# Performance work log

Measured on AMD Instinct MI355X. Metric: run time of the kernel, lower is better.

The kernel has to match this reference:

```python
import jax, jax.numpy as jnp
import numpy as np

B, L, E, H = 4, 2048, 512, 8
D = E // H
FACTOR = 5
U = min(FACTOR * int(np.ceil(np.log(L))), L)  # sample_k == n_top == 40


def setup_inputs() -> dict:
    key0 = jax.random.key(0)
    ks = jax.random.split(key0, 12)
    s = 0.02
    inp = {
        "query": jax.random.normal(ks[0], (B, L, E), jnp.float32),
        "key": jax.random.normal(ks[1], (B, L, E), jnp.float32),
        "value": jax.random.normal(ks[2], (B, L, E), jnp.float32),
        "index_sample": jax.random.randint(ks[3], (L, U), 0, L, jnp.int32),
    }
    for i, nm in enumerate(["q", "k", "v", "o"]):
        inp[f"W{nm}"] = jax.random.normal(ks[4 + i], (E, E), jnp.float32) * s
        inp[f"b{nm}"] = jnp.zeros((E,), jnp.float32)
    return inp


def reference(query, key, value, index_sample, Wq, bq, Wk, bk, Wv, bv, Wo, bo):
    # projections (nn.Linear: x @ W.T + b)
    q = (query @ Wq.T + bq).reshape(B, L, H, D).transpose(0, 2, 1, 3)  # [B,H,L,D]
    k = (key @ Wk.T + bk).reshape(B, L, H, D).transpose(0, 2, 1, 3)
    v = (value @ Wv.T + bv).reshape(B, L, H, D).transpose(0, 2, 1, 3)

    L_Q = L_K = L
    sample_k = index_sample.shape[1]
    n_top = min(sample_k, L_Q)

    # --- _prob_QK: sampled QK scores, note: NO 1/sqrt(D) scaling in source ---
    K_sample = k[:, :, index_sample, :]                      # [B,H,L_Q,sample_k,D]
    QK_sample = jnp.einsum('bhld,bhlsd->bhls', q, K_sample)  # [B,H,L_Q,sample_k]
    M = QK_sample.max(axis=-1) - QK_sample.sum(axis=-1) / L_K
    _, M_top = jax.lax.top_k(M, n_top)                       # [B,H,n_top]
    Q_reduce = jnp.take_along_axis(q, M_top[..., None], axis=2)  # [B,H,n_top,D]
    scores = jnp.einsum('bhud,bhkd->bhuk', Q_reduce, k)      # [B,H,n_top,L_K]

    # --- initial context (eval mode: mean of V) ---
    context = jnp.broadcast_to(v.mean(axis=2, keepdims=True), (B, H, L_Q, D))

    # --- update context at selected queries ---
    attn = jax.nn.softmax(scores, axis=-1)
    upd = jnp.einsum('bhuk,bhkd->bhud', attn, v)             # [B,H,n_top,D]
    bi = jnp.arange(B)[:, None, None]
    hi = jnp.arange(H)[None, :, None]
    context = context.at[bi, hi, M_top].set(upd)

    out = context.transpose(0, 2, 1, 3).reshape(B, L, E) @ Wo.T + bo
    return out
```

## Files before the change

kernel.cpp:

```cpp
#include <hip/hip_runtime.h>
#include <hip/hip_bf16.h>
#include <math.h>

constexpr int BB = 4;
constexpr int LL = 2048;
constexpr int EE = 512;
constexpr int HH = 8;
constexpr int DD = 64;
constexpr int UU = 40;
constexpr int NT = 40;
constexpr int NCH = 32;
constexpr int CK = 64;
constexpr int MVC = 16;
constexpr float NEG_INF = -3.0e38f;

typedef __attribute__((ext_vector_type(8))) short bf8_t;
typedef __attribute__((ext_vector_type(4))) float f4_t;

__device__ __forceinline__ void split2(float x, uint& h, uint& m)
{
    uint  xb = __float_as_uint(x);
    uint  hb = (xb + 0x7fffu + ((xb >> 16) & 1u)) & 0xffff0000u;
    float r  = x - __uint_as_float(hb);
    h = hb >> 16;
    m = (__float_as_uint(r) & 0xffff0000u) >> 16;
}

__device__ __forceinline__ void split2pair(float x0, float x1, uint& hp, uint& mp)
{
    uint xb0 = __float_as_uint(x0), xb1 = __float_as_uint(x1);
    uint hb0 = xb0 + 0x7fffu + ((xb0 >> 16) & 1u);
    uint hb1 = xb1 + 0x7fffu + ((xb1 >> 16) & 1u);
    hp = __builtin_amdgcn_perm(hb1, hb0, 0x07060302u);
    float r0 = x0 - __uint_as_float(hb0 & 0xffff0000u);
    float r1 = x1 - __uint_as_float(hb1 & 0xffff0000u);
    mp = __builtin_amdgcn_perm(__float_as_uint(r1), __float_as_uint(r0), 0x07060302u);
}

__device__ __forceinline__ void gload16(const void* g, void* l)
{
    __builtin_amdgcn_global_load_lds(
        (const __attribute__((address_space(1))) unsigned int*)g,
        (__attribute__((address_space(3))) unsigned int*)l, 16, 0, 0);
}

__device__ __forceinline__ int swz(int row, int c)
{
    return row * 64 + (((c ^ row ^ (row >> 2)) & 3) << 4);
}

__global__ __launch_bounds__(256) void wconv_kernel(
    const float* __restrict__ Wq, const float* __restrict__ Wk,
    const float* __restrict__ Wv, unsigned short* __restrict__ wcv)
{
    const int gi  = blockIdx.x * 256 + threadIdx.x;
    const int z   = gi >> 15;
    const int off = (gi & 32767) * 8;
    const float* W = (z == 0) ? Wq : (z == 1 ? Wk : Wv);
    float x[8];
    *(float4*)(x)     = *(const float4*)(W + off);
    *(float4*)(x + 4) = *(const float4*)(W + off + 4);
    uint hp[4], mp[4];
#pragma unroll
    for (int p = 0; p < 4; p++) split2pair(x[2 * p], x[2 * p + 1], hp[p], mp[p]);
    unsigned short* Wh = wcv + (size_t)z * 524288;
    *(uint4*)(Wh + off)          = make_uint4(hp[0], hp[1], hp[2], hp[3]);
    *(uint4*)(Wh + 262144 + off) = make_uint4(mp[0], mp[1], mp[2], mp[3]);
}

__global__ __launch_bounds__(256, 3) void proj_kernel(
    const float* __restrict__ Xq, const float* __restrict__ Xk, const float* __restrict__ Xv,
    const unsigned short* __restrict__ Wcv,
    const float* __restrict__ bq, const float* __restrict__ bk, const float* __restrict__ bv,
    float* __restrict__ Oq, float* __restrict__ Ok, float* __restrict__ Ov)
{
    const int bid = blockIdx.x;
    const int xg  = bid & 7;
    const int s   = bid >> 3;
    const int yz  = xg * 24 + (s >> 2);
    const int zi  = yz >> 6;
    const int yi  = yz & 63;
    const int m0  = yi * 128;
    const int n0  = (s & 3) * 128;

    const float* X; const float* bias; float* O;
    if (zi == 0)      { X = Xq; bias = bq; O = Oq; }
    else if (zi == 1) { X = Xk; bias = bk; O = Ok; }
    else              { X = Xv; bias = bv; O = Ov; }
    const unsigned short* Wh = Wcv + (size_t)zi * 524288;
    const unsigned short* Wm = Wh + 262144;

    __shared__ char ldsmem[49152];
    char* const LA = ldsmem;
    char* const LB = ldsmem + 16384;

    const int tid  = threadIdx.x;
    const int lane = tid & 63;
    const int wave = tid >> 6;

    const int srow  = tid >> 1;
    const int shalf = tid & 1;
    const int w0 = swz(srow, shalf * 2);
    const int w1 = swz(srow, shalf * 2 + 1);
    const float* Aptr = X + (size_t)(m0 + srow) * EE + shalf * 16;

    const int r0 = tid >> 2;
    const int r1 = 64 + r0;
    const int c0 = (tid & 3) ^ ((r0 ^ (r0 >> 2)) & 3);
    const int c1 = (tid & 3) ^ ((r1 ^ (r1 >> 2)) & 3);
    const unsigned short* bh0 = Wh + (size_t)(n0 + r0) * EE + c0 * 8;
    const unsigned short* bh1 = Wh + (size_t)(n0 + r1) * EE + c1 * 8;
    const unsigned short* bm0 = Wm + (size_t)(n0 + r0) * EE + c0 * 8;
    const unsigned short* bm1 = Wm + (size_t)(n0 + r1) * EE + c1 * 8;
    const int ldst = tid * 16;

    const int rxor = ((((lane >> 4) ^ lane ^ (lane >> 2)) & 3) << 4);
    const int arow = (wave >> 1) * 64 + (lane & 15);
    const int brow = (wave & 1) * 64 + (lane & 15);

    f4_t acc[4][4];
#pragma unroll
    for (int i = 0; i < 4; i++)
#pragma unroll
        for (int j = 0; j < 4; j++) acc[i][j] = (f4_t)0.0f;

    float fa[16];
#pragma unroll
    for (int q = 0; q < 4; q++)
        *(float4*)(fa + q * 4) = *(const float4*)(Aptr + q * 4);
    gload16(bh0, LB + ldst);
    gload16(bh1, LB + 4096 + ldst);
    gload16(bm0, LB + 8192 + ldst);
    gload16(bm1, LB + 12288 + ldst);

    int parity = 0;
#pragma unroll 2
    for (int kt = 0; kt < EE; kt += 32) {
        uint ahu[8], amu[8];
#pragma unroll
        for (int p = 0; p < 8; p++)
            split2pair(fa[2 * p], fa[2 * p + 1], ahu[p], amu[p]);

        __syncthreads();
        *(uint4*)(LA +    0 + w0) = make_uint4(ahu[0], ahu[1], ahu[2], ahu[3]);
        *(uint4*)(LA +    0 + w1) = make_uint4(ahu[4], ahu[5], ahu[6], ahu[7]);
        *(uint4*)(LA + 8192 + w0) = make_uint4(amu[0], amu[1], amu[2], amu[3]);
        *(uint4*)(LA + 8192 + w1) = make_uint4(amu[4], amu[5], amu[6], amu[7]);
        __syncthreads();

        if (kt + 32 < EE) {
            const int kn = kt + 32;
#pragma unroll
            for (int q = 0; q < 4; q++)
                *(float4*)(fa + q * 4) = *(const float4*)(Aptr + kn + q * 4);
            char* Bn = LB + (parity ^ 1) * 16384;
            gload16(bh0 + kn, Bn + ldst);
            gload16(bh1 + kn, Bn + 4096 + ldst);
            gload16(bm0 + kn, Bn + 8192 + ldst);
            gload16(bm1 + kn, Bn + 12288 + ldst);
        }

        char* const Bb = LB + parity * 16384;
        bf8_t af[4][2];
#pragma unroll
        for (int i = 0; i < 4; i++) {
            const int ro = (arow + i * 16) * 64 + rxor;
            af[i][0] = *(const bf8_t*)(LA +    0 + ro);
            af[i][1] = *(const bf8_t*)(LA + 8192 + ro);
        }
#pragma unroll
        for (int j = 0; j < 4; j++) {
            const int ro = (brow + j * 16) * 64 + rxor;
            bf8_t bh_ = *(const bf8_t*)(Bb +    0 + ro);
            bf8_t bm_ = *(const bf8_t*)(Bb + 8192 + ro);
#pragma unroll
            for (int i = 0; i < 4; i++) {
                f4_t c = acc[i][j];
                c = __builtin_amdgcn_mfma_f32_16x16x32_bf16(af[i][0], bh_, c, 0, 0, 0);
                c = __builtin_amdgcn_mfma_f32_16x16x32_bf16(af[i][0], bm_, c, 0, 0, 0);
                c = __builtin_amdgcn_mfma_f32_16x16x32_bf16(af[i][1], bh_, c, 0, 0, 0);
                acc[i][j] = c;
            }
        }
        parity ^= 1;
    }

#pragma unroll
    for (int j = 0; j < 4; j++) {
        const int n  = n0 + (wave & 1) * 64 + j * 16 + (lane & 15);
        const float bn = bias[n];
        const int h_ = n >> 6, d_ = n & 63;
#pragma unroll
        for (int i = 0; i < 4; i++) {
            const int mb = m0 + (wave >> 1) * 64 + i * 16 + ((lane >> 4) << 2);
#pragma unroll
            for (int r = 0; r < 4; r++) {
                const int m  = mb + r;
                const int b_ = m >> 11;
                const int l_ = m & (LL - 1);
                O[(((size_t)(b_ * HH + h_) * LL + l_) << 6) + d_] = acc[i][j][r] + bn;
            }
        }
    }
}

__global__ __launch_bounds__(256) void meanv_part_kernel(const float* __restrict__ v,
                                                         float* __restrict__ vpart)
{
    const int bh    = blockIdx.x & 31;
    const int chunk = blockIdx.x >> 5;
    const int d  = threadIdx.x & 63;
    const int wv = threadIdx.x >> 6;
    const float* base = v + ((size_t)bh * LL + chunk * 128 + wv * 32) * DD + d;
    float acc = 0.0f;
#pragma unroll
    for (int i = 0; i < 32; i++) acc += base[i * DD];
    __shared__ float red[4][DD];
    red[wv][d] = acc;
    __syncthreads();
    if (wv == 0)
        vpart[(size_t)(chunk * 32 + bh) * DD + d]
            = red[0][d] + red[1][d] + red[2][d] + red[3][d];
}

__global__ __launch_bounds__(64) void meanv_comb_kernel(const float* __restrict__ vpart,
                                                        float* __restrict__ mean_v)
{
    const int bh = blockIdx.x;
    const int d  = threadIdx.x;
    float s = 0.0f;
#pragma unroll
    for (int c = 0; c < MVC; c++) s += vpart[(size_t)(c * 32 + bh) * DD + d];
    mean_v[bh * DD + d] = s * (1.0f / (float)LL);
}

__global__ __launch_bounds__(256) void measure_kernel(const float* __restrict__ q,
                                                      const float* __restrict__ k,
                                                      const int* __restrict__ idx_sample,
                                                      float* __restrict__ M)
{
    int bh   = blockIdx.x & 31;
    int lc   = blockIdx.x >> 5;
    int lane = threadIdx.x & 63;
    int wv   = threadIdx.x >> 6;
    int l    = lc * 4 + wv;
    int s8   = lane >> 3;
    int c    = lane & 7;

    const float* qrow = q + ((size_t)bh * LL + l) * DD + c * 8;
    float4 q0 = *(const float4*)(qrow);
    float4 q1 = *(const float4*)(qrow + 4);

    const float* kbase = k + (size_t)bh * LL * DD;
    const int*   irow  = idx_sample + l * UU;

    float mx = NEG_INF, sum = 0.0f;
#pragma unroll
    for (int it = 0; it < UU; it += 8) {
        int ki = irow[it + s8];
        const float* krow = kbase + (size_t)ki * DD + c * 8;
        float4 k0 = *(const float4*)(krow);
        float4 k1 = *(const float4*)(krow + 4);
        float p = q0.x*k0.x + q0.y*k0.y + q0.z*k0.z + q0.w*k0.w
                + q1.x*k1.x + q1.y*k1.y + q1.z*k1.z + q1.w*k1.w;
        p += __shfl_xor(p, 1, 64);
        p += __shfl_xor(p, 2, 64);
        p += __shfl_xor(p, 4, 64);
        mx = fmaxf(mx, p);
        sum += p;
    }
    mx  = fmaxf(mx, __shfl_xor(mx, 8, 64));
    sum += __shfl_xor(sum, 8, 64);
    mx  = fmaxf(mx, __shfl_xor(mx, 16, 64));
    sum += __shfl_xor(sum, 16, 64);
    mx  = fmaxf(mx, __shfl_xor(mx, 32, 64));
    sum += __shfl_xor(sum, 32, 64);

    if (lane == 0) M[bh * LL + l] = mx - sum * (1.0f / (float)LL);
}

__global__ __launch_bounds__(64) void topk_kernel(const float* __restrict__ M,
                                                  int* __restrict__ top)
{
    const int bh   = blockIdx.x;
    const int lane = threadIdx.x;

    unsigned long long keys[32];
#pragma unroll
    for (int i = 0; i < 32; i++) {
        int idx = i * 64 + lane;
        uint u  = __float_as_uint(M[bh * LL + idx]);
        uint sv = (u & 0x80000000u) ? ~u : (u | 0x80000000u);
        keys[i] = ((unsigned long long)sv << 32) | (uint)(LL - 1 - idx);
    }
    unsigned long long lmax = 0ull;
#pragma unroll
    for (int i = 0; i < 32; i++) lmax = (keys[i] > lmax) ? keys[i] : lmax;

    for (int it = 0; it < NT; it++) {
        unsigned long long g = lmax;
#pragma unroll
        for (int off = 1; off < 64; off <<= 1) {
            unsigned long long o = __shfl_xor(g, off, 64);
            g = (o > g) ? o : g;
        }
        if (lane == 0) top[bh * NT + it] = LL - 1 - (int)(g & 0xffffffffu);
#pragma unroll
        for (int i = 0; i < 32; i++) if (keys[i] == g) keys[i] = 0ull;
        lmax = 0ull;
#pragma unroll
        for (int i = 0; i < 32; i++) lmax = (keys[i] > lmax) ? keys[i] : lmax;
    }
}

__global__ __launch_bounds__(256) void pv_kernel(const float* __restrict__ q,
                                                 const float* __restrict__ k,
                                                 const float* __restrict__ v,
                                                 const int* __restrict__ top,
                                                 float* __restrict__ mpart,
                                                 float* __restrict__ lpart,
                                                 float* __restrict__ accpart)
{
    const int bh    = blockIdx.x & 31;
    const int chunk = blockIdx.x >> 5;
    const int tid   = threadIdx.x;
    const int lane  = tid & 63, wv = tid >> 6;

    __shared__ alignas(16) float qs[NT][DD];
    __shared__ alignas(16) float sc[NT][CK + 4];

    for (int i = tid; i < NT * DD / 4; i += 256) {
        int u  = i >> 4;
        int d4 = (i & 15) * 4;
        int l  = top[bh * NT + u];
        *(float4*)&qs[u][d4] = *(const float4*)(q + ((size_t)bh * LL + l) * DD + d4);
    }
    __syncthreads();

    {
        const int key  = tid >> 2;
        const int dseg = tid & 3;
        const float* krow = k + ((size_t)bh * LL + chunk * CK + key) * DD + dseg * 16;
        float4 k0 = *(const float4*)(krow);
        float4 k1 = *(const float4*)(krow + 4);
        float4 k2 = *(const float4*)(krow + 8);
        float4 k3 = *(const float4*)(krow + 12);
#pragma unroll 8
        for (int u = 0; u < NT; u++) {
            const float* qrow = &qs[u][dseg * 16];
            float4 q0 = *(const float4*)(qrow);
            float4 q1 = *(const float4*)(qrow + 4);
            float4 q2 = *(const float4*)(qrow + 8);
            float4 q3 = *(const float4*)(qrow + 12);
            float p = k0.x*q0.x + k0.y*q0.y + k0.z*q0.z + k0.w*q0.w
                    + k1.x*q1.x + k1.y*q1.y + k1.z*q1.z + k1.w*q1.w
                    + k2.x*q2.x + k2.y*q2.y + k2.z*q2.z + k2.w*q2.w
                    + k3.x*q3.x + k3.y*q3.y + k3.z*q3.z + k3.w*q3.w;
            p += __shfl_xor(p, 1, 64);
            p += __shfl_xor(p, 2, 64);
            if (dseg == 0) sc[u][key] = p;
        }
    }
    __syncthreads();

#pragma unroll
    for (int i = 0; i < 10; i++) {
        const int u = wv * 10 + i;
        float val = sc[u][lane];
        float mx = val;
        mx = fmaxf(mx, __shfl_xor(mx, 1, 64));
        mx = fmaxf(mx, __shfl_xor(mx, 2, 64));
        mx = fmaxf(mx, __shfl_xor(mx, 4, 64));
        mx = fmaxf(mx, __shfl_xor(mx, 8, 64));
        mx = fmaxf(mx, __shfl_xor(mx, 16, 64));
        mx = fmaxf(mx, __shfl_xor(mx, 32, 64));
        float e = __expf(val - mx);
        sc[u][lane] = e;
        float s = e;
        s += __shfl_xor(s, 1, 64);
        s += __shfl_xor(s, 2, 64);
        s += __shfl_xor(s, 4, 64);
        s += __shfl_xor(s, 8, 64);
        s += __shfl_xor(s, 16, 64);
        s += __shfl_xor(s, 32, 64);
        if (lane == 0) {
            mpart[(bh * NCH + chunk) * NT + u] = mx;
            lpart[(bh * NCH + chunk) * NT + u] = s;
        }
    }
    __syncthreads();

    {
        float pacc[10];
#pragma unroll
        for (int i = 0; i < 10; i++) pacc[i] = 0.0f;
        const float* vbase = v + ((size_t)bh * LL + chunk * CK) * DD + lane;
#pragma unroll 4
        for (int t = 0; t < CK; t += 4) {
            float v0 = vbase[(size_t)(t + 0) * DD];
            float v1 = vbase[(size_t)(t + 1) * DD];
            float v2 = vbase[(size_t)(t + 2) * DD];
            float v3 = vbase[(size_t)(t + 3) * DD];
#pragma unroll
            for (int i = 0; i < 10; i++) {
                float4 s = *(const float4*)&sc[wv * 10 + i][t];
                pacc[i] += s.x * v0 + s.y * v1 + s.z * v2 + s.w * v3;
            }
        }
#pragma unroll
        for (int i = 0; i < 10; i++) {
            const int u = wv * 10 + i;
            accpart[(((size_t)(bh * NCH + chunk)) * NT + u) * 64 + lane] = pacc[i];
        }
    }
}

__global__ __launch_bounds__(256) void base_kernel(const float* __restrict__ mean_v,
                                                   const float* __restrict__ Wo,
                                                   const float* __restrict__ bo,
                                                   float* __restrict__ base)
{
    int lane = threadIdx.x & 63, wv = threadIdx.x >> 6;
    int be = blockIdx.x * 4 + wv;
    int b  = be >> 9;
    int e  = be & (EE - 1);
    const float* mrow = mean_v + b * EE;
    const float* wrow = Wo + (size_t)e * EE;
    float acc = 0.0f;
#pragma unroll
    for (int j = 0; j < 8; j++) acc += mrow[lane + j * 64] * wrow[lane + j * 64];
#pragma unroll
    for (int off = 32; off > 0; off >>= 1) acc += __shfl_down(acc, off, 64);
    if (lane == 0) base[be] = acc + bo[e];
}

__global__ __launch_bounds__(256) void bcast_kernel(const float* __restrict__ base,
                                                    float* __restrict__ out)
{
    size_t fi = ((size_t)blockIdx.x * 256 + threadIdx.x) * 4;
    int b  = (int)(fi >> 20);
    int e4 = (int)(fi & (EE - 1));
    float4 val = *(const float4*)(base + b * EE + e4);
    *(float4*)(out + fi) = val;
}

__global__ __launch_bounds__(256) void corr_kernel(const float* __restrict__ accpart,
                                                   const float* __restrict__ lpart,
                                                   const float* __restrict__ mpart,
                                                   const float* __restrict__ mean_v,
                                                   const int* __restrict__ top,
                                                   const float* __restrict__ Wo,
                                                   float* __restrict__ out)
{
    int bhu = blockIdx.x;
    int bh  = bhu / NT;
    int u   = bhu % NT;
    int h   = bh & (HH - 1);
    int b   = bh >> 3;
    int tid = threadIdx.x;
    int l   = top[bhu];

    __shared__ float delta[DD];
    if (tid < DD) {
        float m = NEG_INF;
#pragma unroll 8
        for (int c = 0; c < NCH; c++) m = fmaxf(m, mpart[(bh * NCH + c) * NT + u]);
        float den = 0.0f, num = 0.0f;
#pragma unroll 8
        for (int c = 0; c < NCH; c++) {
            float f = __expf(mpart[(bh * NCH + c) * NT + u] - m);
            den += lpart[(bh * NCH + c) * NT + u] * f;
            num += accpart[(((size_t)(bh * NCH + c)) * NT + u) * 64 + tid] * f;
        }
        delta[tid] = num / den - mean_v[bh * DD + tid];
    }
    __syncthreads();

    float* orow = out + ((size_t)(b * LL + l)) * EE;
#pragma unroll
    for (int rep = 0; rep < 2; rep++) {
        int e = tid + rep * 256;
        const float* wrow = Wo + (size_t)e * EE + h * DD;
        float acc = 0.0f;
#pragma unroll
        for (int d = 0; d < DD; d++) acc += delta[d] * wrow[d];
        atomicAdd(orow + e, acc);
    }
}

extern "C" void kernel_launch(void* const* d_in, const int* in_sizes, int n_in,
                              void* d_out, int out_size, void* d_ws, size_t ws_size,
                              hipStream_t stream)
{
    const float* query = (const float*)d_in[0];
    const float* key   = (const float*)d_in[1];
    const float* value = (const float*)d_in[2];
    const int*   idxs  = (const int*)d_in[3];
    const float* Wq = (const float*)d_in[4];
    const float* bq = (const float*)d_in[5];
    const float* Wk = (const float*)d_in[6];
    const float* bk = (const float*)d_in[7];
    const float* Wv = (const float*)d_in[8];
    const float* bv = (const float*)d_in[9];
    const float* Wo = (const float*)d_in[10];
    const float* bo = (const float*)d_in[11];
    float* out = (float*)d_out;

    char* ws = (char*)d_ws;
    size_t off = 0;
    const size_t qkv_bytes = (size_t)BB * HH * LL * DD * sizeof(float);
    float* q_ws = (float*)(ws + off); off += qkv_bytes;
    float* k_ws = (float*)(ws + off); off += qkv_bytes;
    float* v_ws = (float*)(ws + off); off += qkv_bytes;
    float* M_ws    = (float*)(ws + off); off += (size_t)BB * HH * LL * sizeof(float);
    int*   top_ws  = (int*)(ws + off);   off += (size_t)BB * HH * NT * sizeof(int);
    float* mean_ws = (float*)(ws + off); off += (size_t)BB * HH * DD * sizeof(float);
    float* vpart_ws = (float*)(ws + off); off += (size_t)BB * HH * MVC * DD * sizeof(float);
    float* mpart_ws = (float*)(ws + off); off += (size_t)BB * HH * NCH * NT * sizeof(float);
    float* lpart_ws = (float*)(ws + off); off += (size_t)BB * HH * NCH * NT * sizeof(float);
    float* accpart_ws = (float*)(ws + off); off += (size_t)BB * HH * NCH * NT * DD * sizeof(float);
    float* base_ws = (float*)(ws + off); off += (size_t)BB * EE * sizeof(float);

    unsigned short* wcv_ws = (unsigned short*)accpart_ws;

    wconv_kernel<<<384, 256, 0, stream>>>(Wq, Wk, Wv, wcv_ws);
    proj_kernel<<<768, 256, 0, stream>>>(query, key, value, wcv_ws, bq, bk, bv,
                                         q_ws, k_ws, v_ws);
    meanv_part_kernel<<<BB * HH * MVC, 256, 0, stream>>>(v_ws, vpart_ws);
    meanv_comb_kernel<<<BB * HH, 64, 0, stream>>>(vpart_ws, mean_ws);
    measure_kernel<<<(LL / 4) * 32, 256, 0, stream>>>(q_ws, k_ws, idxs, M_ws);
    topk_kernel<<<BB * HH, 64, 0, stream>>>(M_ws, top_ws);
    pv_kernel<<<BB * HH * NCH, 256, 0, stream>>>(q_ws, k_ws, v_ws, top_ws,
                                                 mpart_ws, lpart_ws, accpart_ws);
    base_kernel<<<(BB * EE) / 4, 256, 0, stream>>>(mean_ws, Wo, bo, base_ws);
    bcast_kernel<<<(BB * LL * EE) / (256 * 4), 256, 0, stream>>>(base_ws, out);
    corr_kernel<<<BB * HH * NT, 256, 0, stream>>>(accpart_ws, lpart_ws, mpart_ws,
                                                  mean_ws, top_ws, Wo, out);
}
```

Baseline: 316.3 us.

## Double-buffer A tile in LDS and cut to one barrier per K-step

The projection GEMM now double-buffers the converted A tile (bf16 hi/lo split) in LDS alongside B, and prefetches raw A two steps ahead in registers. The A conversion and LDS write for the next step overlap with the MFMAs of the current one. This replaces two __syncthreads per iteration with a single manual waitcnt plus s_barrier. LDS grows to 64KB and launch bounds drop to 2 blocks per CU, which lowers occupancy in exchange for less synchronization stall.

```diff
diff --git a/kernel.cpp b/kernel.cpp
--- a/kernel.cpp
+++ b/kernel.cpp
@@ -17,15 +17,6 @@
 typedef __attribute__((ext_vector_type(8))) short bf8_t;
 typedef __attribute__((ext_vector_type(4))) float f4_t;
 
-__device__ __forceinline__ void split2(float x, uint& h, uint& m)
-{
-    uint  xb = __float_as_uint(x);
-    uint  hb = (xb + 0x7fffu + ((xb >> 16) & 1u)) & 0xffff0000u;
-    float r  = x - __uint_as_float(hb);
-    h = hb >> 16;
-    m = (__float_as_uint(r) & 0xffff0000u) >> 16;
-}
-
 __device__ __forceinline__ void split2pair(float x0, float x1, uint& hp, uint& mp)
 {
     uint xb0 = __float_as_uint(x0), xb1 = __float_as_uint(x1);
@@ -68,7 +59,7 @@
     *(uint4*)(Wh + 262144 + off) = make_uint4(mp[0], mp[1], mp[2], mp[3]);
 }
 
-__global__ __launch_bounds__(256, 3) void proj_kernel(
+__global__ __launch_bounds__(256, 2) void proj_kernel(
     const float* __restrict__ Xq, const float* __restrict__ Xk, const float* __restrict__ Xv,
     const unsigned short* __restrict__ Wcv,
     const float* __restrict__ bq, const float* __restrict__ bk, const float* __restrict__ bv,
@@ -90,9 +81,9 @@
     const unsigned short* Wh = Wcv + (size_t)zi * 524288;
     const unsigned short* Wm = Wh + 262144;
 
-    __shared__ char ldsmem[49152];
-    char* const LA = ldsmem;
-    char* const LB = ldsmem + 16384;
+    __shared__ char ldsmem[65536];
+    char* const LA  = ldsmem;
+    char* const LBt = ldsmem + 32768;
 
     const int tid  = threadIdx.x;
     const int lane = tid & 63;
@@ -124,65 +115,97 @@
 #pragma unroll
         for (int j = 0; j < 4; j++) acc[i][j] = (f4_t)0.0f;
 
-    float fa[16];
-#pragma unroll
-    for (int q = 0; q < 4; q++)
-        *(float4*)(fa + q * 4) = *(const float4*)(Aptr + q * 4);
-    gload16(bh0, LB + ldst);
-    gload16(bh1, LB + 4096 + ldst);
-    gload16(bm0, LB + 8192 + ldst);
-    gload16(bm1, LB + 12288 + ldst);
-
-    int parity = 0;
-#pragma unroll 2
-    for (int kt = 0; kt < EE; kt += 32) {
+    float faA[16], faB[16];
+
+    {
+        float f0[16];
+#pragma unroll
+        for (int q = 0; q < 4; q++)
+            *(float4*)(f0 + q * 4) = *(const float4*)(Aptr + q * 4);
         uint ahu[8], amu[8];
 #pragma unroll
         for (int p = 0; p < 8; p++)
-            split2pair(fa[2 * p], fa[2 * p + 1], ahu[p], amu[p]);
-
-        __syncthreads();
+            split2pair(f0[2 * p], f0[2 * p + 1], ahu[p], amu[p]);
         *(uint4*)(LA +    0 + w0) = make_uint4(ahu[0], ahu[1], ahu[2], ahu[3]);
         *(uint4*)(LA +    0 + w1) = make_uint4(ahu[4], ahu[5], ahu[6], ahu[7]);
         *(uint4*)(LA + 8192 + w0) = make_uint4(amu[0], amu[1], amu[2], amu[3]);
         *(uint4*)(LA + 8192 + w1) = make_uint4(amu[4], amu[5], amu[6], amu[7]);
-        __syncthreads();
-
-        if (kt + 32 < EE) {
-            const int kn = kt + 32;
+        gload16(bh0, LBt + ldst);
+        gload16(bh1, LBt + 4096 + ldst);
+        gload16(bm0, LBt + 8192 + ldst);
+        gload16(bm1, LBt + 12288 + ldst);
+        asm volatile("" ::: "memory");
+#pragma unroll
+        for (int q = 0; q < 4; q++)
+            *(float4*)(faB + q * 4) = *(const float4*)(Aptr + 32 + q * 4);
+        asm volatile("s_waitcnt vmcnt(4) lgkmcnt(0)" ::: "memory");
+        __builtin_amdgcn_s_barrier();
+    }
+
+    auto body = [&](int i, float* fconv, float* fload) {
+        char* const Ab = LA  + ((i & 1) << 14);
+        char* const Bb = LBt + ((i & 1) << 14);
+
+        bf8_t af[4][2];
+#pragma unroll
+        for (int i4 = 0; i4 < 4; i4++) {
+            const int ro = (arow + i4 * 16) * 64 + rxor;
+            af[i4][0] = *(const bf8_t*)(Ab +    0 + ro);
+            af[i4][1] = *(const bf8_t*)(Ab + 8192 + ro);
+        }
+
+        if (i < 15) {
+            uint ahu[8], amu[8];
+#pragma unroll
+            for (int p = 0; p < 8; p++)
+                split2pair(fconv[2 * p], fconv[2 * p + 1], ahu[p], amu[p]);
+            char* const Aw = LA + (((i + 1) & 1) << 14);
+            *(uint4*)(Aw +    0 + w0) = make_uint4(ahu[0], ahu[1], ahu[2], ahu[3]);
+            *(uint4*)(Aw +    0 + w1) = make_uint4(ahu[4], ahu[5], ahu[6], ahu[7]);
+            *(uint4*)(Aw + 8192 + w0) = make_uint4(amu[0], amu[1], amu[2], amu[3]);
+            *(uint4*)(Aw + 8192 + w1) = make_uint4(amu[4], amu[5], amu[6], amu[7]);
+            const int kn = (i + 1) * 32;
+            char* const Bw = LBt + (((i + 1) & 1) << 14);
+            gload16(bh0 + kn, Bw + ldst);
+            gload16(bh1 + kn, Bw + 4096 + ldst);
+            gload16(bm0 + kn, Bw + 8192 + ldst);
+            gload16(bm1 + kn, Bw + 12288 + ldst);
+        }
+        asm volatile("" ::: "memory");
+        if (i < 14) {
+            const int kf = (i + 2) * 32;
 #pragma unroll
             for (int q = 0; q < 4; q++)
-                *(float4*)(fa + q * 4) = *(const float4*)(Aptr + kn + q * 4);
-            char* Bn = LB + (parity ^ 1) * 16384;
-            gload16(bh0 + kn, Bn + ldst);
-            gload16(bh1 + kn, Bn + 4096 + ldst);
-            gload16(bm0 + kn, Bn + 8192 + ldst);
-            gload16(bm1 + kn, Bn + 12288 + ldst);
-        }
-
-        char* const Bb = LB + parity * 16384;
-        bf8_t af[4][2];
-#pragma unroll
-        for (int i = 0; i < 4; i++) {
-            const int ro = (arow + i * 16) * 64 + rxor;
-            af[i][0] = *(const bf8_t*)(LA +    0 + ro);
-            af[i][1] = *(const bf8_t*)(LA + 8192 + ro);
-        }
+                *(float4*)(fload + q * 4) = *(const float4*)(Aptr + kf + q * 4);
+        }
+
 #pragma unroll
         for (int j = 0; j < 4; j++) {
             const int ro = (brow + j * 16) * 64 + rxor;
             bf8_t bh_ = *(const bf8_t*)(Bb +    0 + ro);
             bf8_t bm_ = *(const bf8_t*)(Bb + 8192 + ro);
 #pragma unroll
-            for (int i = 0; i < 4; i++) {
-                f4_t c = acc[i][j];
-                c = __builtin_amdgcn_mfma_f32_16x16x32_bf16(af[i][0], bh_, c, 0, 0, 0);
-                c = __builtin_amdgcn_mfma_f32_16x16x32_bf16(af[i][0], bm_, c, 0, 0, 0);
-                c = __builtin_amdgcn_mfma_f32_16x16x32_bf16(af[i][1], bh_, c, 0, 0, 0);
-                acc[i][j] = c;
+            for (int i4 = 0; i4 < 4; i4++) {
+                f4_t c = acc[i4][j];
+                c = __builtin_amdgcn_mfma_f32_16x16x32_bf16(af[i4][0], bh_, c, 0, 0, 0);
+                c = __builtin_amdgcn_mfma_f32_16x16x32_bf16(af[i4][0], bm_, c, 0, 0, 0);
+                c = __builtin_amdgcn_mfma_f32_16x16x32_bf16(af[i4][1], bh_, c, 0, 0, 0);
+                acc[i4][j] = c;
             }
         }
-        parity ^= 1;
+
+        if (i < 15) {
+            if (i < 14)
+                asm volatile("s_waitcnt vmcnt(4) lgkmcnt(0)" ::: "memory");
+            else
+                asm volatile("s_waitcnt vmcnt(0) lgkmcnt(0)" ::: "memory");
+            __builtin_amdgcn_s_barrier();
+        }
+    };
+
+    for (int it = 0; it < 16; it += 2) {
+        body(it,     faB, faA);
+        body(it + 1, faA, faB);
     }
 
 #pragma unroll
```

Result: no change. 321.6 us (+1.7%).

## Restructure correction kernel to reuse Wo tile across all selected queries per head

Applied to the files above, without the earlier changes.

The correction kernel now runs one block per (batch-head, 128-column slice of output) instead of one block per selected query. Each block combines the partial softmax results for all 40 selected queries into shared memory and stages a 128x64 slice of Wo in LDS, so each Wo element is read once per head rather than once per query. The grid shrinks from 1280 to 128 blocks, which lowers parallelism and adds redundant recombination of partials across the four column slices. The PV inner loop is also changed from a float4 step over four keys to scalar per-key loads with unroll 8.

```diff
diff --git a/kernel.cpp b/kernel.cpp
--- a/kernel.cpp
+++ b/kernel.cpp
@@ -16,15 +16,6 @@
 
 typedef __attribute__((ext_vector_type(8))) short bf8_t;
 typedef __attribute__((ext_vector_type(4))) float f4_t;
-
-__device__ __forceinline__ void split2(float x, uint& h, uint& m)
-{
-    uint  xb = __float_as_uint(x);
-    uint  hb = (xb + 0x7fffu + ((xb >> 16) & 1u)) & 0xffff0000u;
-    float r  = x - __uint_as_float(hb);
-    h = hb >> 16;
-    m = (__float_as_uint(r) & 0xffff0000u) >> 16;
-}
 
 __device__ __forceinline__ void split2pair(float x0, float x1, uint& hp, uint& mp)
 {
@@ -326,8 +317,8 @@
     const int tid   = threadIdx.x;
     const int lane  = tid & 63, wv = tid >> 6;
 
-    __shared__ alignas(16) float qs[NT][DD];
-    __shared__ alignas(16) float sc[NT][CK + 4];
+    __shared__ float qs[NT][DD];
+    __shared__ float sc[NT][CK + 4];
 
     for (int i = tid; i < NT * DD / 4; i += 256) {
         int u  = i >> 4;
@@ -394,18 +385,12 @@
         float pacc[10];
 #pragma unroll
         for (int i = 0; i < 10; i++) pacc[i] = 0.0f;
-        const float* vbase = v + ((size_t)bh * LL + chunk * CK) * DD + lane;
-#pragma unroll 4
-        for (int t = 0; t < CK; t += 4) {
-            float v0 = vbase[(size_t)(t + 0) * DD];
-            float v1 = vbase[(size_t)(t + 1) * DD];
-            float v2 = vbase[(size_t)(t + 2) * DD];
-            float v3 = vbase[(size_t)(t + 3) * DD];
-#pragma unroll
-            for (int i = 0; i < 10; i++) {
-                float4 s = *(const float4*)&sc[wv * 10 + i][t];
-                pacc[i] += s.x * v0 + s.y * v1 + s.z * v2 + s.w * v3;
-            }
+        const float* vbase = v + ((size_t)bh * LL + chunk * CK) * DD;
+#pragma unroll 8
+        for (int t = 0; t < CK; t++) {
+            float vval = vbase[(size_t)t * DD + lane];
+#pragma unroll
+            for (int i = 0; i < 10; i++) pacc[i] += sc[wv * 10 + i][t] * vval;
         }
 #pragma unroll
         for (int i = 0; i < 10; i++) {
@@ -452,39 +437,56 @@
                                                    const float* __restrict__ Wo,
                                                    float* __restrict__ out)
 {
-    int bhu = blockIdx.x;
-    int bh  = bhu / NT;
-    int u   = bhu % NT;
-    int h   = bh & (HH - 1);
-    int b   = bh >> 3;
-    int tid = threadIdx.x;
-    int l   = top[bhu];
-
-    __shared__ float delta[DD];
-    if (tid < DD) {
-        float m = NEG_INF;
+    const int bh  = blockIdx.x & 31;
+    const int ec  = blockIdx.x >> 5;
+    const int h   = bh & (HH - 1);
+    const int b   = bh >> 3;
+    const int tid = threadIdx.x;
+
+    __shared__ float delta[NT][DD + 1];
+    __shared__ float wot[128][DD + 1];
+    __shared__ int   ltab[NT];
+
+    {
+        const int ug = tid >> 6;
+        const int d  = tid & 63;
+        for (int u = ug; u < NT; u += 4) {
+            const float* mp = mpart + (size_t)bh * NCH * NT + u;
+            const float* lp = lpart + (size_t)bh * NCH * NT + u;
+            float m = NEG_INF;
 #pragma unroll 8
-        for (int c = 0; c < NCH; c++) m = fmaxf(m, mpart[(bh * NCH + c) * NT + u]);
-        float den = 0.0f, num = 0.0f;
+            for (int c = 0; c < NCH; c++) m = fmaxf(m, mp[c * NT]);
+            float den = 0.0f, num = 0.0f;
 #pragma unroll 8
-        for (int c = 0; c < NCH; c++) {
-            float f = __expf(mpart[(bh * NCH + c) * NT + u] - m);
-            den += lpart[(bh * NCH + c) * NT + u] * f;
-            num += accpart[(((size_t)(bh * NCH + c)) * NT + u) * 64 + tid] * f;
-        }
-        delta[tid] = num / den - mean_v[bh * DD + tid];
+            for (int c = 0; c < NCH; c++) {
+                float f = __expf(mp[c * NT] - m);
+                den += lp[c * NT] * f;
+                num += accpart[(((size_t)(bh * NCH + c)) * NT + u) * 64 + d] * f;
+            }
+            delta[u][d] = num / den - mean_v[bh * DD + d];
+        }
+    }
+    if (tid < NT) ltab[tid] = top[bh * NT + tid];
+
+    const int e0 = ec * 128;
+#pragma unroll
+    for (int p = 0; p < 8; p++) {
+        const int r  = p * 16 + (tid >> 4);
+        const int c4 = (tid & 15) * 4;
+        *(float4*)&wot[r][c4] = *(const float4*)(Wo + (size_t)(e0 + r) * EE + h * DD + c4);
     }
     __syncthreads();
 
-    float* orow = out + ((size_t)(b * LL + l)) * EE;
-#pragma unroll
-    for (int rep = 0; rep < 2; rep++) {
-        int e = tid + rep * 256;
-        const float* wrow = Wo + (size_t)e * EE + h * DD;
+    const int el = tid >> 1;
+    const int u0 = (tid & 1) * 20;
+    float* orowbase = out + (size_t)b * LL * EE + e0 + el;
+#pragma unroll 4
+    for (int uu = 0; uu < 20; uu++) {
+        const int u = u0 + uu;
         float acc = 0.0f;
 #pragma unroll
-        for (int d = 0; d < DD; d++) acc += delta[d] * wrow[d];
-        atomicAdd(orow + e, acc);
+        for (int d = 0; d < DD; d++) acc += delta[u][d] * wot[el][d];
+        atomicAdd(orowbase + (size_t)ltab[u] * EE, acc);
     }
 }
 
@@ -534,6 +536,6 @@
                                                  mpart_ws, lpart_ws, accpart_ws);
     base_kernel<<<(BB * EE) / 4, 256, 0, stream>>>(mean_ws, Wo, bo, base_ws);
     bcast_kernel<<<(BB * LL * EE) / (256 * 4), 256, 0, stream>>>(base_ws, out);
-    corr_kernel<<<BB * HH * NT, 256, 0, stream>>>(accpart_ws, lpart_ws, mpart_ws,
-                                                  mean_ws, top_ws, Wo, out);
-}
+    corr_kernel<<<128, 256, 0, stream>>>(accpart_ws, lpart_ws, mpart_ws,
+                                         mean_ws, top_ws, Wo, out);
+}
```

Result: no change. 312.8 us (-1.1%).
